# Optimization experiments

Hardware: AMD Instinct MI355X
Metric: run time of the kernel (lower is better)

Reference implementation:

```python
import jax, jax.numpy as jnp
import numpy as np
from jax import lax

NS, W, BS, NSENT, EMB, H, NMEN, NCAND, NTOK, NENTV = 640, 64, 16, 40, 512, 256, 32, 32, 50000, 100000


def _gru_dir(xp, valid, Whh, bhh):
    # xp: [T,B,3H] precomputed input projection; valid: [T,B] bool
    h0 = jnp.zeros((xp.shape[1], Whh.shape[1]), xp.dtype)
    def step(h, inp):
        x, v = inp
        g = h @ Whh.T + bhh
        xr, xz, xn = jnp.split(x, 3, axis=-1)
        hr, hz, hn = jnp.split(g, 3, axis=-1)
        r = jax.nn.sigmoid(xr + hr)
        z = jax.nn.sigmoid(xz + hz)
        n = jnp.tanh(xn + r * hn)
        hnew = (1.0 - z) * n + z * h
        hnew = jnp.where(v[:, None], hnew, h)  # freeze state past seq end (packed-seq semantics)
        return hnew, hnew * v[:, None]         # zero padded outputs like pad_packed_sequence
    _, ys = lax.scan(step, h0, (xp, valid))
    return ys  # [T,B,H]


def _att_birnn(x, lens, Wih_f, Whh_f, bih_f, bhh_f, Wih_b, Whh_b, bih_b, bhh_b, lin_w, lin_b, attw):
    # x: [B,T,I], lens: [B] (descending, lens[0]==T) -> attended pooling [B,2H]
    T = x.shape[1]
    valid = jnp.arange(T)[:, None] < lens[None, :]  # [T,B]
    xp_f = jnp.einsum('bti,oi->tbo', x, Wih_f) + bih_f
    xp_b = jnp.einsum('bti,oi->tbo', x, Wih_b) + bih_b
    ys_f = _gru_dir(xp_f, valid, Whh_f, bhh_f)
    ys_b = _gru_dir(xp_b[::-1], valid[::-1], Whh_b, bhh_b)[::-1]
    enc = jnp.concatenate([ys_f, ys_b], -1)  # [T,B,2H]
    emb_h = jnp.tanh(jnp.einsum('tbh,oh->tbo', enc, lin_w) + lin_b)
    att = emb_h @ attw  # [T,B]
    e = jnp.exp(att) * valid  # original uses raw exp with additive 1e-4 denom
    wgt = e / (jnp.sum(e, 0, keepdims=True) + 1e-4)
    return jnp.sum(wgt[..., None] * enc, 0)  # [B,2H]


def _cos(a, b, eps=1e-8):
    dot = jnp.sum(a * b, -1)
    na = jnp.sqrt(jnp.sum(a * a, -1))
    nb = jnp.sqrt(jnp.sum(b * b, -1))
    return dot / jnp.maximum(na * nb, eps)


def _forward(batch_doc, sent_order, length_sent, length_doc, men_sent_idx, can_ent_idx, cand_mask,
             embed_doc, embed_ent, wp, sp, mlp_w, mlp_b):
    emb_w = embed_doc[batch_doc]                         # [NS,W,EMB]; eval mode -> no dropout
    sent_embs = _att_birnn(emb_w, length_sent, *wp)      # [NS,2H]
    padded = jnp.concatenate([jnp.zeros((1, sent_embs.shape[1]), sent_embs.dtype), sent_embs], 0)
    each_sent = padded[sent_order]                       # [BS,NSENT,2H] (_reorder_sent)
    doc_embs = _att_birnn(each_sent, length_doc, *sp)    # [BS,2H]
    emb_ent = embed_ent[can_ent_idx]                     # [BS,NMEN,NCAND,EMB]
    sent_vecs = each_sent[jnp.arange(each_sent.shape[0])[:, None], men_sent_idx]  # [BS,NMEN,2H]
    # vectorized replacement of the triple python loop of per-element cosine sims
    ss = _cos(sent_vecs[:, :, None, :], emb_ent) * cand_mask  # [BS,NMEN,NCAND]
    ds = _cos(doc_embs[:, None, None, :], emb_ent) * cand_mask
    cc = jnp.concatenate([ss, ds], -1)                   # [BS,NMEN,2*NCAND]
    mask = (ss != 0).astype(cc.dtype)
    return (cc @ mlp_w.T + mlp_b) * mask


def setup_inputs() -> dict:
    key = jax.random.key(0)
    ks = jax.random.split(key, 36)
    batch_doc = jax.random.randint(ks[0], (NS, W), 0, NTOK, dtype=jnp.int32)
    length_sent = jnp.sort(jax.random.randint(ks[1], (NS,), 1, W + 1, dtype=jnp.int32))[::-1].at[0].set(W)
    length_doc = jnp.sort(jax.random.randint(ks[2], (BS,), 1, NSENT + 1, dtype=jnp.int32))[::-1].at[0].set(NSENT)
    so = jax.random.randint(ks[3], (BS, NSENT), 1, NS + 1, dtype=jnp.int32)
    sent_order = jnp.where(jnp.arange(NSENT)[None, :] < length_doc[:, None], so, 0)
    men_sent_idx = jax.random.randint(ks[4], (BS, NMEN), 0, NSENT, dtype=jnp.int32) % length_doc[:, None]
    can_ent_idx = jax.random.randint(ks[5], (BS, NMEN, NCAND), 1, NENTV, dtype=jnp.int32)
    cand_mask = (jax.random.uniform(ks[6], (BS, NMEN, NCAND)) < 0.8).astype(jnp.float32)
    def nrm(k, shape, s=0.05):
        return s * jax.random.normal(k, shape, dtype=jnp.float32)
    embed_doc = nrm(ks[7], (NTOK, EMB)).at[0].set(0.0)   # padding_idx=0
    embed_ent = nrm(ks[8], (NENTV, EMB)).at[0].set(0.0)
    d = {
        'batch_doc': batch_doc, 'sent_order': sent_order, 'length_sent': length_sent,
        'length_doc': length_doc, 'men_sent_idx': men_sent_idx, 'can_ent_idx': can_ent_idx,
        'cand_mask': cand_mask, 'embed_doc': embed_doc, 'embed_ent': embed_ent,
        'w_Wih_f': nrm(ks[9], (3 * H, EMB)), 'w_Whh_f': nrm(ks[10], (3 * H, H)),
        'w_bih_f': nrm(ks[11], (3 * H,)), 'w_bhh_f': nrm(ks[12], (3 * H,)),
        'w_Wih_b': nrm(ks[13], (3 * H, EMB)), 'w_Whh_b': nrm(ks[14], (3 * H, H)),
        'w_bih_b': nrm(ks[15], (3 * H,)), 'w_bhh_b': nrm(ks[16], (3 * H,)),
        'w_lin_w': nrm(ks[17], (2 * H, 2 * H)), 'w_lin_b': nrm(ks[18], (2 * H,)),
        'w_attw': nrm(ks[19], (2 * H,)),
        's_Wih_f': nrm(ks[20], (3 * H, 2 * H)), 's_Whh_f': nrm(ks[21], (3 * H, H)),
        's_bih_f': nrm(ks[22], (3 * H,)), 's_bhh_f': nrm(ks[23], (3 * H,)),
        's_Wih_b': nrm(ks[24], (3 * H, 2 * H)), 's_Whh_b': nrm(ks[25], (3 * H, H)),
        's_bih_b': nrm(ks[26], (3 * H,)), 's_bhh_b': nrm(ks[27], (3 * H,)),
        's_lin_w': nrm(ks[28], (2 * H, 2 * H)), 's_lin_b': nrm(ks[29], (2 * H,)),
        's_attw': nrm(ks[30], (2 * H,)),
        'mlp_w': nrm(ks[31], (NCAND, 2 * NCAND)), 'mlp_b': nrm(ks[32], (NCAND,)),
    }
    return d


def reference(batch_doc, sent_order, length_sent, length_doc, men_sent_idx, can_ent_idx, cand_mask,
              embed_doc, embed_ent,
              w_Wih_f, w_Whh_f, w_bih_f, w_bhh_f, w_Wih_b, w_Whh_b, w_bih_b, w_bhh_b, w_lin_w, w_lin_b, w_attw,
              s_Wih_f, s_Whh_f, s_bih_f, s_bhh_f, s_Wih_b, s_Whh_b, s_bih_b, s_bhh_b, s_lin_w, s_lin_b, s_attw,
              mlp_w, mlp_b):
    wp = (w_Wih_f, w_Whh_f, w_bih_f, w_bhh_f, w_Wih_b, w_Whh_b, w_bih_b, w_bhh_b, w_lin_w, w_lin_b, w_attw)
    sp = (s_Wih_f, s_Whh_f, s_bih_f, s_bhh_f, s_Wih_b, s_Whh_b, s_bih_b, s_bhh_b, s_lin_w, s_lin_b, s_attw)
    return _forward(batch_doc, sent_order, length_sent, length_doc, men_sent_idx, can_ent_idx, cand_mask,
                    embed_doc, embed_ent, wp, sp, mlp_w, mlp_b)
```

## Files before the change

### kernel.cpp

```cpp
#include <hip/hip_runtime.h>
#include <cstdint>
#include <cstddef>


typedef __attribute__((ext_vector_type(8))) short bf16x8;
typedef __attribute__((ext_vector_type(8))) _Float16 f16x8;
typedef __attribute__((ext_vector_type(4))) float f32x4;

__device__ __forceinline__ float bfraw2f(unsigned int u16) {
    unsigned int x = u16 << 16; float f; __builtin_memcpy(&f, &x, 4); return f;
}
__device__ __forceinline__ unsigned short f2bfraw(float f) {
    unsigned int u; __builtin_memcpy(&u, &f, 4);
    unsigned int r = u + 0x7fffu + ((u >> 16) & 1u);
    return (unsigned short)(r >> 16);
}
__device__ __forceinline__ unsigned short f2h(float f) {
    _Float16 h = (_Float16)f; unsigned short u; __builtin_memcpy(&u, &h, 2); return u;
}
__device__ __forceinline__ float h2f(unsigned short u) {
    _Float16 h; __builtin_memcpy(&h, &u, 2); return (float)h;
}
__device__ __forceinline__ float bflo(unsigned int p) {
    unsigned int x = p << 16; float f; __builtin_memcpy(&f, &x, 4); return f;
}
__device__ __forceinline__ float bfhi(unsigned int p) {
    unsigned int x = p & 0xffff0000u; float f; __builtin_memcpy(&f, &x, 4); return f;
}
__device__ __forceinline__ float fast_sigmoid(float x) { return 1.f / (1.f + __expf(-x)); }
__device__ __forceinline__ float fast_tanh(float x) {
    x = fminf(fmaxf(x, -30.f), 30.f);
    float e = __expf(2.f * x);
    return (e - 1.f) / (e + 1.f);
}
__device__ __forceinline__ float fin(float x) {
    return (x == x && fabsf(x) < 1e30f) ? x : 0.f;
}

__device__ __forceinline__ float ldsc(const void* p, size_t i, int m) {
    return m ? bfraw2f(((const unsigned short*)p)[i]) : ((const float*)p)[i];
}
__device__ __forceinline__ bf16x8 ld8bf(const void* p, size_t ei, int m) {
    if (m) return *(const bf16x8*)((const unsigned short*)p + ei);
    const float* f = (const float*)p + ei;
    f32x4 a = *(const f32x4*)f, b = *(const f32x4*)(f + 4);
    bf16x8 r;
    r[0] = (short)f2bfraw(a[0]); r[1] = (short)f2bfraw(a[1]);
    r[2] = (short)f2bfraw(a[2]); r[3] = (short)f2bfraw(a[3]);
    r[4] = (short)f2bfraw(b[0]); r[5] = (short)f2bfraw(b[1]);
    r[6] = (short)f2bfraw(b[2]); r[7] = (short)f2bfraw(b[3]);
    return r;
}
__device__ __forceinline__ void ld8f(const void* p, size_t ei, int m, float* o) {
    if (m) {
        uint4 wv = *(const uint4*)((const unsigned short*)p + ei);
        o[0] = bflo(wv.x); o[1] = bfhi(wv.x); o[2] = bflo(wv.y); o[3] = bfhi(wv.y);
        o[4] = bflo(wv.z); o[5] = bfhi(wv.z); o[6] = bflo(wv.w); o[7] = bfhi(wv.w);
    } else {
        const float* f = (const float*)p + ei;
        #pragma unroll
        for (int i = 0; i < 8; ++i) o[i] = f[i];
    }
}

__global__ void k_probe(const unsigned short* __restrict__ w, int* __restrict__ flag) {
    if (threadIdx.x == 0) {
        int bad = 0;
        for (int i = 0; i < 512; ++i) {
            float v = bfraw2f(w[i]);
            if (!(fabsf(v) <= 1.0f)) bad++;
        }
        flag[0] = (bad == 0) ? 1 : 0;
        flag[1] = 1;
    }
}

__global__ void p_cvt(const void* __restrict__ src, unsigned short* __restrict__ dst,
                      int n, const int* __restrict__ modep) {
    const int m = modep[0];
    for (int i = blockIdx.x * 256 + threadIdx.x; i < n; i += gridDim.x * 256)
        dst[i] = f2bfraw(ldsc(src, i, m));
}
__global__ void p_cvt_h(const void* __restrict__ src, unsigned short* __restrict__ dst,
                        int n, const int* __restrict__ modep) {
    const int m = modep[0];
    for (int i = blockIdx.x * 256 + threadIdx.x; i < n; i += gridDim.x * 256)
        dst[i] = f2h(ldsc(src, i, m));
}

__global__ void p_whh_swz(const void* __restrict__ whh, unsigned short* __restrict__ dst,
                          const int* __restrict__ modep) {
    const int m = modep[0];
    const int idx = blockIdx.x * 256 + threadIdx.x;
    if (idx >= 24576) return;
    const int lane = idx & 63, ks = (idx >> 6) & 7;
    const int g = (idx >> 9) % 6, w = idx / 3072;
    const int lm = lane & 15, q = lane >> 4;
    const int reg = g >> 1, nt = g & 1;
    const int row = reg * 256 + w * 32 + nt * 16 + lm;
    const size_t src = (size_t)row * 256 + ks * 32 + q * 8;
    const size_t d = (size_t)idx * 8;
    #pragma unroll
    for (int e = 0; e < 8; ++e) dst[d + e] = f2bfraw(ldsc(whh, src + e, m));
}

__global__ __launch_bounds__(256, 2) void k_xp_word(
    const void* __restrict__ embA, const int* __restrict__ batch_doc,
    const unsigned short* __restrict__ wih,
    const void* __restrict__ bih_f, const void* __restrict__ bih_b,
    unsigned short* __restrict__ xp, int b0, int nb,
    const int* __restrict__ amode, const int* __restrict__ modep)
{
    __shared__ unsigned short As[64][40];
    __shared__ unsigned short Bs[256][40];
    const int am = amode[0], m = modep[0];
    const int bm = blockIdx.x, bc = blockIdx.y;
    const int tid = threadIdx.x;
    const int wave = tid >> 6, lane = tid & 63, lm = lane & 15, q = lane >> 4;
    const int arow = tid >> 2, akoff = (tid & 3) * 8;
    const int r = bm * 64 + arow;
    const int tt = r / nb, bl = r - tt * nb;
    const size_t aei = (size_t)batch_doc[(b0 + bl) * 64 + tt] * 512 + akoff;

    const f32x4 fzero = {0.f, 0.f, 0.f, 0.f};
    f32x4 acc[4][4];
    #pragma unroll
    for (int i = 0; i < 4; ++i)
        #pragma unroll
        for (int j = 0; j < 4; ++j) acc[i][j] = fzero;

    for (int kt = 0; kt < 16; ++kt) {
        *(bf16x8*)&As[arow][akoff] = ld8bf(embA, aei + kt * 32, am);
        #pragma unroll
        for (int ld = 0; ld < 4; ++ld) {
            int e = ld * 256 + tid;
            int n = e >> 2, koff = (e & 3) * 8;
            int gn = bc * 256 + n;
            *(uint4*)&Bs[n][koff] = *(const uint4*)(wih + (size_t)gn * 512 + kt * 32 + koff);
        }
        __syncthreads();
        bf16x8 af[4], bv[4];
        #pragma unroll
        for (int mt = 0; mt < 4; ++mt) af[mt] = *(const bf16x8*)&As[mt * 16 + lm][q * 8];
        #pragma unroll
        for (int nt = 0; nt < 4; ++nt) bv[nt] = *(const bf16x8*)&Bs[wave * 64 + nt * 16 + lm][q * 8];
        #pragma unroll
        for (int mt = 0; mt < 4; ++mt)
            #pragma unroll
            for (int nt = 0; nt < 4; ++nt)
                acc[mt][nt] = __builtin_amdgcn_mfma_f32_16x16x32_bf16(af[mt], bv[nt], acc[mt][nt], 0, 0, 0);
        __syncthreads();
    }

    const size_t XPT = (size_t)64 * nb * 768;
    #pragma unroll
    for (int nt = 0; nt < 4; ++nt) {
        const int cn = bc * 256 + wave * 64 + nt * 16 + lm;
        const int dirb = (cn >= 768);
        const int o = cn - dirb * 768;
        const float bias = ldsc(dirb ? bih_b : bih_f, o, m);
        #pragma unroll
        for (int mt = 0; mt < 4; ++mt)
            #pragma unroll
            for (int j = 0; j < 4; ++j) {
                const int rr = bm * 64 + mt * 16 + q * 4 + j;
                xp[(dirb ? XPT : 0) + (size_t)rr * 768 + o] = f2h(acc[mt][nt][j] + bias);
            }
    }
}

__global__ __launch_bounds__(512, 2) void k_gru(
    const unsigned short* __restrict__ xp,
    const unsigned short* __restrict__ wswz_f,
    const unsigned short* __restrict__ wswz_b,
    const void* __restrict__ bhh_f, const void* __restrict__ bhh_b,
    const int* __restrict__ lens, unsigned short* __restrict__ enc, int T, int NB,
    const int* __restrict__ modep)
{
    __shared__ unsigned short hHi[2][16][264];
    __shared__ unsigned short hLo[2][16][264];
    __shared__ unsigned short xpS[2][16][776];
    __shared__ float bhhS[768];
    __shared__ int lensS[16];
    const int m = modep[0];
    const int tid = threadIdx.x;
    const int w = tid >> 6, lane = tid & 63, lm = lane & 15, q = lane >> 4;
    const int dir = blockIdx.x & 1, sg = blockIdx.x >> 1;
    const int s0 = sg << 4;
    const unsigned short* wsw =
        (dir ? wswz_b : wswz_f) + (size_t)w * 24576 + (size_t)lane * 8;
    const void* bhh = dir ? bhh_b : bhh_f;
    const unsigned short* xpd = xp + (dir ? (size_t)T * NB * 768 : 0);

    for (int e = tid; e < 16 * 264; e += 512) {
        (&hHi[0][0][0])[e] = 0; (&hLo[0][0][0])[e] = 0;
    }
    for (int j = tid; j < 768; j += 512) bhhS[j] = ldsc(bhh, j, m);
    if (tid < 16) lensS[tid] = lens[s0 + tid];

    bf16x8 bper[3][8];
    #pragma unroll
    for (int g = 0; g < 3; ++g)
        #pragma unroll
        for (int ks = 0; ks < 8; ++ks)
            bper[g][ks] = *(const bf16x8*)(wsw + (size_t)(g * 8 + ks) * 512);

    {
        const int t0 = dir ? (T - 1) : 0;
        const unsigned short* xrow = xpd + ((size_t)t0 * NB + s0) * 768;
        #pragma unroll
        for (int i = 0; i < 3; ++i) {
            int e = tid + i * 512;
            uint4 v = *(const uint4*)(xrow + e * 8);
            *(uint4*)&xpS[0][e / 96][(e % 96) * 8] = v;
        }
    }
    __syncthreads();

    const f32x4 fzero = {0.f, 0.f, 0.f, 0.f};
    float hreg[2][4] = {};
    uint4 stg[3];
    for (int step = 0; step < T; ++step) {
        const int t = dir ? (T - 1 - step) : step;
        const int cur = step & 1, nxt = cur ^ 1;

        const bool havenext = (step + 1 < T);
        if (havenext) {
            const int tn = dir ? (T - 2 - step) : (step + 1);
            const unsigned short* xrow = xpd + ((size_t)tn * NB + s0) * 768;
            #pragma unroll
            for (int i = 0; i < 3; ++i)
                stg[i] = *(const uint4*)(xrow + (tid + i * 512) * 8);
        }

        f32x4 acc[6];
        #pragma unroll
        for (int i = 0; i < 6; ++i) acc[i] = fzero;

        #pragma unroll
        for (int ph = 0; ph < 2; ++ph) {
            const int kb = ph * 4;
            bf16x8 ahi[4], alo[4];
            #pragma unroll
            for (int k = 0; k < 4; ++k) {
                ahi[k] = *(const bf16x8*)&hHi[cur][lm][(kb + k) * 32 + q * 8];
                alo[k] = *(const bf16x8*)&hLo[cur][lm][(kb + k) * 32 + q * 8];
            }
            bf16x8 bs3[4], bs4[4], bs5[4];
            #pragma unroll
            for (int k = 0; k < 4; ++k) {
                bs3[k] = *(const bf16x8*)(wsw + (size_t)(24 + kb + k) * 512);
                bs4[k] = *(const bf16x8*)(wsw + (size_t)(32 + kb + k) * 512);
                bs5[k] = *(const bf16x8*)(wsw + (size_t)(40 + kb + k) * 512);
            }
            #pragma unroll
            for (int g = 0; g < 3; ++g)
                #pragma unroll
                for (int k = 0; k < 4; ++k) {
                    acc[g] = __builtin_amdgcn_mfma_f32_16x16x32_bf16(ahi[k], bper[g][kb + k], acc[g], 0, 0, 0);
                    acc[g] = __builtin_amdgcn_mfma_f32_16x16x32_bf16(alo[k], bper[g][kb + k], acc[g], 0, 0, 0);
                }
            #pragma unroll
            for (int k = 0; k < 4; ++k) {
                acc[3] = __builtin_amdgcn_mfma_f32_16x16x32_bf16(ahi[k], bs3[k], acc[3], 0, 0, 0);
                acc[3] = __builtin_amdgcn_mfma_f32_16x16x32_bf16(alo[k], bs3[k], acc[3], 0, 0, 0);
                acc[4] = __builtin_amdgcn_mfma_f32_16x16x32_bf16(ahi[k], bs4[k], acc[4], 0, 0, 0);
                acc[4] = __builtin_amdgcn_mfma_f32_16x16x32_bf16(alo[k], bs4[k], acc[4], 0, 0, 0);
                acc[5] = __builtin_amdgcn_mfma_f32_16x16x32_bf16(ahi[k], bs5[k], acc[5], 0, 0, 0);
                acc[5] = __builtin_amdgcn_mfma_f32_16x16x32_bf16(alo[k], bs5[k], acc[5], 0, 0, 0);
            }
        }

        #pragma unroll
        for (int nt = 0; nt < 2; ++nt) {
            const int col = w * 32 + nt * 16 + lm;
            const float br = bhhS[col], bz = bhhS[256 + col], bn = bhhS[512 + col];
            #pragma unroll
            for (int j = 0; j < 4; ++j) {
                const int s = q * 4 + j;
                const float xr = h2f(xpS[cur][s][col]);
                const float xz = h2f(xpS[cur][s][256 + col]);
                const float xn = h2f(xpS[cur][s][512 + col]);
                const float rr = fast_sigmoid(xr + acc[nt][j] + br);
                const float zz = fast_sigmoid(xz + acc[2 + nt][j] + bz);
                const float nn = fast_tanh(xn + rr * (acc[4 + nt][j] + bn));
                const float hold = hreg[nt][j];
                float hnew = (1.f - zz) * nn + zz * hold;
                const bool v = (t < lensS[s]);
                hnew = v ? hnew : hold;
                hreg[nt][j] = hnew;
                const unsigned short uh = f2bfraw(hnew);
                hHi[nxt][s][col] = uh;
                hLo[nxt][s][col] = f2bfraw(hnew - bfraw2f(uh));
                enc[((size_t)t * NB + s0 + s) * 512 + (size_t)dir * 256 + col] = f2h(v ? hnew : 0.f);
            }
        }

        if (havenext) {
            #pragma unroll
            for (int i = 0; i < 3; ++i) {
                int e = tid + i * 512;
                *(uint4*)&xpS[nxt][e / 96][(e % 96) * 8] = stg[i];
            }
        }
        __syncthreads();
    }
}

__global__ __launch_bounds__(256, 1) void k_att(
    const unsigned short* __restrict__ enc,
    const unsigned short* __restrict__ lin_w,
    const void* __restrict__ lin_b, const void* __restrict__ attw,
    float* __restrict__ att_out, const int* __restrict__ modep)
{
    __shared__ unsigned short As[64][40];
    __shared__ unsigned short Bs[512][40];
    __shared__ float att_part[4][64];
    const int m = modep[0];
    const int bm = blockIdx.x;
    const int tid = threadIdx.x;
    const int wave = tid >> 6, lane = tid & 63, lm = lane & 15, q = lane >> 4;
    const int arow = tid >> 2, akoff = (tid & 3) * 8;
    const unsigned short* aptr = enc + (size_t)(bm * 64 + arow) * 512 + akoff;

    const f32x4 fzero = {0.f, 0.f, 0.f, 0.f};
    f32x4 acc[4][8];
    #pragma unroll
    for (int i = 0; i < 4; ++i)
        #pragma unroll
        for (int j = 0; j < 8; ++j) acc[i][j] = fzero;

    for (int kt = 0; kt < 16; ++kt) {
        *(uint4*)&As[arow][akoff] = *(const uint4*)(aptr + kt * 32);
        #pragma unroll
        for (int ld = 0; ld < 8; ++ld) {
            int e = ld * 256 + tid;
            int n = e >> 2, koff = (e & 3) * 8;
            *(uint4*)&Bs[n][koff] = *(const uint4*)(lin_w + (size_t)n * 512 + kt * 32 + koff);
        }
        __syncthreads();
        f16x8 af[4];
        #pragma unroll
        for (int mt = 0; mt < 4; ++mt) af[mt] = *(const f16x8*)&As[mt * 16 + lm][q * 8];
        #pragma unroll
        for (int nt = 0; nt < 8; ++nt) {
            f16x8 bv = *(const f16x8*)&Bs[wave * 128 + nt * 16 + lm][q * 8];
            #pragma unroll
            for (int mt = 0; mt < 4; ++mt)
                acc[mt][nt] = __builtin_amdgcn_mfma_f32_16x16x32_f16(af[mt], bv, acc[mt][nt], 0, 0, 0);
        }
        __syncthreads();
    }

    float part[4][4] = {};
    #pragma unroll
    for (int nt = 0; nt < 8; ++nt) {
        const int col = wave * 128 + nt * 16 + lm;
        const float lb = ldsc(lin_b, col, m);
        const float aw = ldsc(attw, col, m);
        #pragma unroll
        for (int mt = 0; mt < 4; ++mt)
            #pragma unroll
            for (int j = 0; j < 4; ++j)
                part[mt][j] += fast_tanh(acc[mt][nt][j] + lb) * aw;
    }
    #pragma unroll
    for (int mt = 0; mt < 4; ++mt)
        #pragma unroll
        for (int j = 0; j < 4; ++j) {
            float v = part[mt][j];
            #pragma unroll
            for (int d0 = 1; d0 < 16; d0 <<= 1) v += __shfl_xor(v, d0);
            part[mt][j] = v;
        }
    if (lm == 0) {
        #pragma unroll
        for (int mt = 0; mt < 4; ++mt)
            #pragma unroll
            for (int j = 0; j < 4; ++j)
                att_part[wave][mt * 16 + q * 4 + j] = part[mt][j];
    }
    __syncthreads();
    if (tid < 64)
        att_out[(size_t)bm * 64 + tid] =
            att_part[0][tid] + att_part[1][tid] + att_part[2][tid] + att_part[3][tid];
}

__global__ __launch_bounds__(256) void k_softsum(
    const float* __restrict__ att, const unsigned short* __restrict__ enc,
    const int* __restrict__ lens, float* __restrict__ out,
    float* __restrict__ zero_row, int T, int NB)
{
    __shared__ float eS[64];
    __shared__ float dS;
    const int bb = blockIdx.x, tid = threadIdx.x;
    if (zero_row && bb == 0) { for (int j = tid; j < 512; j += 256) zero_row[j] = 0.f; }
    const int len = lens[bb];
    if (tid < T) {
        float a = fminf(att[(size_t)tid * NB + bb], 50.f);
        eS[tid] = (tid < len) ? __expf(a) : 0.f;
    }
    __syncthreads();
    if (tid == 0) { float s = 0.f; for (int t2 = 0; t2 < T; ++t2) s += eS[t2]; dS = s + 1e-4f; }
    __syncthreads();
    const float inv = 1.f / dS;
    for (int j = tid; j < 512; j += 256) {
        float a0 = 0.f;
        for (int t2 = 0; t2 < T; ++t2) a0 += eS[t2] * h2f(enc[((size_t)t2 * NB + bb) * 512 + j]);
        out[(size_t)bb * 512 + j] = fin(a0 * inv);
    }
}

__global__ __launch_bounds__(256) void k_sent_xp(
    const int* __restrict__ sent_order, const float* __restrict__ sent_pad,
    const unsigned short* __restrict__ swih,
    const void* __restrict__ bih_f, const void* __restrict__ bih_b,
    float* __restrict__ each_sent, unsigned short* __restrict__ xp_s,
    const int* __restrict__ modep)
{
    __shared__ float aS[512];
    const int m = modep[0];
    const int r = blockIdx.x, tid = threadIdx.x;
    const int idx = sent_order[r];
    const float* src = sent_pad + (size_t)idx * 512;
    for (int j = tid; j < 512; j += 256) { float v = src[j]; aS[j] = v; each_sent[(size_t)r * 512 + j] = v; }
    __syncthreads();
    const int d = r / 40, i2 = r % 40;
    #pragma unroll
    for (int p = 0; p < 6; ++p) {
        const int o = p * 256 + tid;
        const int dirb = (o >= 768);
        const int oo = o - dirb * 768;
        float s = ldsc(dirb ? bih_b : bih_f, oo, m);
        const unsigned short* wrow = swih + (size_t)o * 512;
        for (int k = 0; k < 512; k += 8) {
            const uint4 wv = *(const uint4*)(wrow + k);
            float wf[8];
            wf[0] = bflo(wv.x); wf[1] = bfhi(wv.x); wf[2] = bflo(wv.y); wf[3] = bfhi(wv.y);
            wf[4] = bflo(wv.z); wf[5] = bfhi(wv.z); wf[6] = bflo(wv.w); wf[7] = bfhi(wv.w);
            #pragma unroll
            for (int u = 0; u < 8; ++u) s += aS[k + u] * wf[u];
        }
        xp_s[(size_t)dirb * (40 * 16 * 768) + ((size_t)i2 * 16 + d) * 768 + oo] = f2h(s);
    }
}

__global__ __launch_bounds__(256) void k_final(
    const int* __restrict__ men_sent_idx, const int* __restrict__ can_ent_idx,
    const void* __restrict__ cand_mask, const void* __restrict__ embed_ent,
    const float* __restrict__ each_sent, const float* __restrict__ doc_embs,
    const void* __restrict__ mlp_w, const void* __restrict__ mlp_b,
    void* __restrict__ out, const int* __restrict__ modep)
{
    const int bm = blockIdx.x;
    const int b = bm >> 5;
    __shared__ float sv[512], dv[512];
    __shared__ float red[256];
    __shared__ float ssA[32], dsA[32];
    __shared__ float norms[2];
    const int m = modep[0];
    const int tid = threadIdx.x;
    const int sidx = men_sent_idx[bm];
    const float* svp = each_sent + ((size_t)b * 40 + sidx) * 512;
    const float* dvp = doc_embs + (size_t)b * 512;
    float pa = 0.f, pd = 0.f;
    for (int j = tid; j < 512; j += 256) {
        float a = svp[j], d0 = dvp[j];
        sv[j] = a; dv[j] = d0; pa += a * a; pd += d0 * d0;
    }
    red[tid] = pa; __syncthreads();
    for (int s = 128; s > 0; s >>= 1) { if (tid < s) red[tid] += red[tid + s]; __syncthreads(); }
    if (tid == 0) norms[0] = sqrtf(red[0]);
    __syncthreads();
    red[tid] = pd; __syncthreads();
    for (int s = 128; s > 0; s >>= 1) { if (tid < s) red[tid] += red[tid + s]; __syncthreads(); }
    if (tid == 0) norms[1] = sqrtf(red[0]);
    __syncthreads();

    const int c = tid >> 3, jg = tid & 7;
    const int ei = can_ent_idx[(size_t)bm * 32 + c];
    float dsv = 0.f, ddv = 0.f, ne = 0.f;
    for (int k = 0; k < 64; k += 8) {
        float wf[8];
        ld8f(embed_ent, (size_t)ei * 512 + jg * 64 + k, m, wf);
        const int base = jg * 64 + k;
        #pragma unroll
        for (int u = 0; u < 8; ++u) {
            dsv += sv[base + u] * wf[u];
            ddv += dv[base + u] * wf[u];
            ne  += wf[u] * wf[u];
        }
    }
    #pragma unroll
    for (int d0 = 1; d0 < 8; d0 <<= 1) {
        dsv += __shfl_xor(dsv, d0);
        ddv += __shfl_xor(ddv, d0);
        ne  += __shfl_xor(ne, d0);
    }
    if (jg == 0) {
        const float nen = sqrtf(ne);
        const float cm = ldsc(cand_mask, (size_t)bm * 32 + c, m);
        ssA[c] = dsv / fmaxf(norms[0] * nen, 1e-8f) * cm;
        dsA[c] = ddv / fmaxf(norms[1] * nen, 1e-8f) * cm;
    }
    __syncthreads();
    if (tid < 32) {
        float o = ldsc(mlp_b, tid, m);
        for (int j2 = 0; j2 < 32; ++j2) {
            o += ssA[j2] * ldsc(mlp_w, tid * 64 + j2, m);
            o += dsA[j2] * ldsc(mlp_w, tid * 64 + 32 + j2, m);
        }
        const float maskv = (ssA[tid] != 0.f) ? 1.f : 0.f;
        const float v = fin(o * maskv);
        if (m) ((unsigned short*)out)[(size_t)bm * 32 + tid] = f2bfraw(v);
        else   ((float*)out)[(size_t)bm * 32 + tid] = v;
    }
}

extern "C" void kernel_launch(void* const* d_in, const int* in_sizes, int n_in,
                              void* d_out, int out_size, void* d_ws, size_t ws_size,
                              hipStream_t stream)
{
    (void)in_sizes; (void)n_in; (void)out_size;
    const int* batch_doc    = (const int*)d_in[0];
    const int* sent_order   = (const int*)d_in[1];
    const int* length_sent  = (const int*)d_in[2];
    const int* length_doc   = (const int*)d_in[3];
    const int* men_sent_idx = (const int*)d_in[4];
    const int* can_ent_idx  = (const int*)d_in[5];
    const void* cand_mask = d_in[6];
    const void* embed_doc = d_in[7];
    const void* embed_ent = d_in[8];
    const void* wWihF = d_in[9];
    const void* wWhhF = d_in[10];
    const void* wBihF = d_in[11];
    const void* wBhhF = d_in[12];
    const void* wWihB = d_in[13];
    const void* wWhhB = d_in[14];
    const void* wBihB = d_in[15];
    const void* wBhhB = d_in[16];
    const void* wLinW = d_in[17];
    const void* wLinB = d_in[18];
    const void* wAttw = d_in[19];
    const void* sWihF = d_in[20];
    const void* sWhhF = d_in[21];
    const void* sBihF = d_in[22];
    const void* sBhhF = d_in[23];
    const void* sWihB = d_in[24];
    const void* sWhhB = d_in[25];
    const void* sBihB = d_in[26];
    const void* sBhhB = d_in[27];
    const void* sLinW = d_in[28];
    const void* sLinB = d_in[29];
    const void* sAttw = d_in[30];
    const void* mlpW  = d_in[31];
    const void* mlpB  = d_in[32];

    const size_t N_EMB = (size_t)50000 * 512;
    const size_t HEAD =
        256 + 4 * (size_t)196608 * 2 +
        (size_t)1536 * 512 * 2 + (size_t)512 * 512 * 2 +
        (size_t)1536 * 512 * 2 + (size_t)512 * 512 * 2 +
        (size_t)328192 * 4;
    const size_t SENT_REGION = 1310720 + 1966080 + 655360 + 2816 + 32768;
    auto need = [&](int nbq, int e) -> size_t {
        size_t word = (size_t)nbq * (196608 + 65536 + 256);
        size_t region = word > SENT_REGION ? word : SENT_REGION;
        return HEAD + region + (e ? N_EMB * 2 : 0) + (1u << 20);
    };
    int emb_cvt = 1, nb = 320;
    {
        const int ladder[6] = {640, 320, 160, 80, 40, 16};
        bool found = false;
        for (int i = 0; i < 6 && !found; ++i)
            for (int e = 1; e >= 0 && !found; --e)
                if (need(ladder[i], e) <= ws_size) { emb_cvt = e; nb = ladder[i]; found = true; }
    }

    char* base = (char*)d_ws;
    size_t off = 0;
    auto take = [&](size_t bytes) -> void* {
        void* p = base + off; off += (bytes + 255) & ~(size_t)255; return p;
    };
    int* mode = (int*)take(256);
    unsigned short* swzWF = (unsigned short*)take((size_t)196608 * 2);
    unsigned short* swzWB = (unsigned short*)take((size_t)196608 * 2);
    unsigned short* swzSF = (unsigned short*)take((size_t)196608 * 2);
    unsigned short* swzSB = (unsigned short*)take((size_t)196608 * 2);
    unsigned short* wih_w = (unsigned short*)take((size_t)1536 * 512 * 2);
    unsigned short* lin_h = (unsigned short*)take((size_t)512 * 512 * 2);
    unsigned short* swih  = (unsigned short*)take((size_t)1536 * 512 * 2);
    unsigned short* slin_h= (unsigned short*)take((size_t)512 * 512 * 2);
    float* sent_pad  = (float*)take((size_t)328192 * 4);

    size_t word_bytes = (size_t)nb * (196608 + 65536 + 256);
    size_t region_bytes = word_bytes > SENT_REGION ? word_bytes : SENT_REGION;
    char* region = (char*)take(region_bytes);
    unsigned short* xp_c  = (unsigned short*)region;
    unsigned short* enc_c = (unsigned short*)(region + (size_t)nb * 196608);
    float* att_c          = (float*)(region + (size_t)nb * 196608 + (size_t)nb * 65536);
    float* each_sent      = (float*)region;
    unsigned short* xp_s  = (unsigned short*)(region + 1310720);
    unsigned short* enc_s = (unsigned short*)(region + 1310720 + 1966080);
    float* att_s          = (float*)(region + 1310720 + 1966080 + 655360);
    float* doc_embs       = (float*)(region + 1310720 + 1966080 + 655360 + 2816);

    unsigned short* emb_bf = emb_cvt ? (unsigned short*)take(N_EMB * 2) : nullptr;

    k_probe<<<1, 64, 0, stream>>>((const unsigned short*)wWhhF, mode);
    p_whh_swz<<<96, 256, 0, stream>>>(wWhhF, swzWF, mode);
    p_whh_swz<<<96, 256, 0, stream>>>(wWhhB, swzWB, mode);
    p_whh_swz<<<96, 256, 0, stream>>>(sWhhF, swzSF, mode);
    p_whh_swz<<<96, 256, 0, stream>>>(sWhhB, swzSB, mode);
    p_cvt<<<256, 256, 0, stream>>>(wWihF, wih_w, 768 * 512, mode);
    p_cvt<<<256, 256, 0, stream>>>(wWihB, wih_w + (size_t)768 * 512, 768 * 512, mode);
    p_cvt_h<<<256, 256, 0, stream>>>(wLinW, lin_h, 512 * 512, mode);
    p_cvt<<<256, 256, 0, stream>>>(sWihF, swih, 768 * 512, mode);
    p_cvt<<<256, 256, 0, stream>>>(sWihB, swih + (size_t)768 * 512, 768 * 512, mode);
    p_cvt_h<<<256, 256, 0, stream>>>(sLinW, slin_h, 512 * 512, mode);
    if (emb_cvt) p_cvt<<<2048, 256, 0, stream>>>(embed_doc, emb_bf, (int)N_EMB, mode);

    const void* embA = emb_cvt ? (const void*)emb_bf : embed_doc;
    const int* amode = emb_cvt ? (mode + 1) : mode;

    for (int b0 = 0; b0 < 640; b0 += nb) {
        k_xp_word<<<dim3(nb, 6), 256, 0, stream>>>(embA, batch_doc, wih_w,
                                                   wBihF, wBihB, xp_c, b0, nb, amode, mode);
        k_gru<<<2 * (nb / 16), 512, 0, stream>>>(xp_c, swzWF, swzWB, wBhhF, wBhhB,
                                                 length_sent + b0, enc_c, 64, nb, mode);
        k_att<<<nb, 256, 0, stream>>>(enc_c, lin_h, wLinB, wAttw, att_c, mode);
        k_softsum<<<nb, 256, 0, stream>>>(att_c, enc_c, length_sent + b0,
                                          sent_pad + (size_t)(1 + b0) * 512,
                                          (b0 == 0) ? sent_pad : nullptr, 64, nb);
    }
    k_sent_xp<<<640, 256, 0, stream>>>(sent_order, sent_pad, swih, sBihF, sBihB,
                                       each_sent, xp_s, mode);
    k_gru<<<2, 512, 0, stream>>>(xp_s, swzSF, swzSB, sBhhF, sBhhB,
                                 length_doc, enc_s, 40, 16, mode);
    k_att<<<10, 256, 0, stream>>>(enc_s, slin_h, sLinB, sAttw, att_s, mode);
    k_softsum<<<16, 256, 0, stream>>>(att_s, enc_s, length_doc, doc_embs, nullptr, 40, 16);
    k_final<<<512, 256, 0, stream>>>(men_sent_idx, can_ent_idx, cand_mask, embed_ent,
                                     each_sent, doc_embs, mlpW, mlpB, d_out, mode);
}
```

Baseline: 1.385 ms.

## Add single-pass workspace plan that skips embedding-table conversion and aliases buffers

```diff
diff --git a/kernel.cpp b/kernel.cpp
--- a/kernel.cpp
+++ b/kernel.cpp
@@ -557,6 +557,68 @@
     const void* mlpB  = d_in[32];
 
     const size_t N_EMB = (size_t)50000 * 512;
+    char* base = (char*)d_ws;
+
+    const size_t SP_MODE  = 0;
+    const size_t SP_SWZWF = 256;
+    const size_t SP_SWZWB = SP_SWZWF + 393216;
+    const size_t SP_ATTC  = SP_SWZWB + 393216;
+    const size_t SP_XPC   = SP_ATTC + 163840;
+    const size_t SP_ENCC  = SP_XPC + (size_t)125829120;
+    const size_t SP_END   = SP_ENCC + (size_t)41943040;
+    const bool single = (SP_END + 65536) <= ws_size;
+
+    if (single) {
+        int* mode             = (int*)(base + SP_MODE);
+        unsigned short* swzWF = (unsigned short*)(base + SP_SWZWF);
+        unsigned short* swzWB = (unsigned short*)(base + SP_SWZWB);
+        float* att_c          = (float*)(base + SP_ATTC);
+        unsigned short* xp_c  = (unsigned short*)(base + SP_XPC);
+        unsigned short* enc_c = (unsigned short*)(base + SP_ENCC);
+        unsigned short* wih_w = enc_c;
+        char* xr = (char*)xp_c;
+        unsigned short* lin_h  = (unsigned short*)(xr);
+        float* sent_pad        = (float*)(xr + 524288);
+        unsigned short* swzSF  = (unsigned short*)(xr + 1837056);
+        unsigned short* swzSB  = (unsigned short*)(xr + 2230272);
+        unsigned short* swih   = (unsigned short*)(xr + 2623488);
+        unsigned short* slin_h = (unsigned short*)(xr + 4196352);
+        float* each_sent       = (float*)(xr + 4720640);
+        unsigned short* xp_s   = (unsigned short*)(xr + 6031360);
+        unsigned short* enc_s  = (unsigned short*)(xr + 7997440);
+        float* att_s           = (float*)(xr + 8652800);
+        float* doc_embs        = (float*)(xr + 8655616);
+
+        k_probe<<<1, 64, 0, stream>>>((const unsigned short*)wWhhF, mode);
+        p_whh_swz<<<96, 256, 0, stream>>>(wWhhF, swzWF, mode);
+        p_whh_swz<<<96, 256, 0, stream>>>(wWhhB, swzWB, mode);
+        p_cvt<<<256, 256, 0, stream>>>(wWihF, wih_w, 768 * 512, mode);
+        p_cvt<<<256, 256, 0, stream>>>(wWihB, wih_w + (size_t)768 * 512, 768 * 512, mode);
+
+        k_xp_word<<<dim3(640, 6), 256, 0, stream>>>(embed_doc, batch_doc, wih_w,
+                                                    wBihF, wBihB, xp_c, 0, 640, mode, mode);
+        k_gru<<<80, 512, 0, stream>>>(xp_c, swzWF, swzWB, wBhhF, wBhhB,
+                                      length_sent, enc_c, 64, 640, mode);
+        p_cvt_h<<<128, 256, 0, stream>>>(wLinW, lin_h, 512 * 512, mode);
+        k_att<<<640, 256, 0, stream>>>(enc_c, lin_h, wLinB, wAttw, att_c, mode);
+        k_softsum<<<640, 256, 0, stream>>>(att_c, enc_c, length_sent,
+                                           sent_pad + 512, sent_pad, 64, 640);
+        p_whh_swz<<<96, 256, 0, stream>>>(sWhhF, swzSF, mode);
+        p_whh_swz<<<96, 256, 0, stream>>>(sWhhB, swzSB, mode);
+        p_cvt<<<256, 256, 0, stream>>>(sWihF, swih, 768 * 512, mode);
+        p_cvt<<<256, 256, 0, stream>>>(sWihB, swih + (size_t)768 * 512, 768 * 512, mode);
+        p_cvt_h<<<128, 256, 0, stream>>>(sLinW, slin_h, 512 * 512, mode);
+        k_sent_xp<<<640, 256, 0, stream>>>(sent_order, sent_pad, swih, sBihF, sBihB,
+                                           each_sent, xp_s, mode);
+        k_gru<<<2, 512, 0, stream>>>(xp_s, swzSF, swzSB, sBhhF, sBhhB,
+                                     length_doc, enc_s, 40, 16, mode);
+        k_att<<<10, 256, 0, stream>>>(enc_s, slin_h, sLinB, sAttw, att_s, mode);
+        k_softsum<<<16, 256, 0, stream>>>(att_s, enc_s, length_doc, doc_embs, nullptr, 40, 16);
+        k_final<<<512, 256, 0, stream>>>(men_sent_idx, can_ent_idx, cand_mask, embed_ent,
+                                         each_sent, doc_embs, mlpW, mlpB, d_out, mode);
+        return;
+    }
+
     const size_t HEAD =
         256 + 4 * (size_t)196608 * 2 +
         (size_t)1536 * 512 * 2 + (size_t)512 * 512 * 2 +
@@ -570,14 +632,13 @@
     };
     int emb_cvt = 1, nb = 320;
     {
-        const int ladder[6] = {640, 320, 160, 80, 40, 16};
+        const int ladder[5] = {320, 160, 80, 40, 16};
         bool found = false;
-        for (int i = 0; i < 6 && !found; ++i)
+        for (int i = 0; i < 5 && !found; ++i)
             for (int e = 1; e >= 0 && !found; --e)
                 if (need(ladder[i], e) <= ws_size) { emb_cvt = e; nb = ladder[i]; found = true; }
     }
 
-    char* base = (char*)d_ws;
     size_t off = 0;
     auto take = [&](size_t bytes) -> void* {
         void* p = base + off; off += (bytes + 255) & ~(size_t)255; return p;
```

After: 1.359 ms. No clear change (-1.9%).

## Switch GRU recurrence to single fp16 MFMA and pre-swizzle input projections

Applied to the files above, without the earlier changes.

```diff
diff --git a/kernel.cpp b/kernel.cpp
--- a/kernel.cpp
+++ b/kernel.cpp
@@ -101,7 +101,7 @@
     const size_t src = (size_t)row * 256 + ks * 32 + q * 8;
     const size_t d = (size_t)idx * 8;
     #pragma unroll
-    for (int e = 0; e < 8; ++e) dst[d + e] = f2bfraw(ldsc(whh, src + e, m));
+    for (int e = 0; e < 8; ++e) dst[d + e] = f2h(ldsc(whh, src + e, m));
 }
 
 __global__ __launch_bounds__(256, 2) void k_xp_word(
@@ -153,18 +153,28 @@
     }
 
     const size_t XPT = (size_t)64 * nb * 768;
+    const int nbg = nb >> 4;
     #pragma unroll
     for (int nt = 0; nt < 4; ++nt) {
         const int cn = bc * 256 + wave * 64 + nt * 16 + lm;
         const int dirb = (cn >= 768);
         const int o = cn - dirb * 768;
         const float bias = ldsc(dirb ? bih_b : bih_f, o, m);
+        const int gate = o >> 8, c = o & 255;
+        const int ww = c >> 5, ntt = (c >> 4) & 1, lmm = c & 15;
+        const int u0 = gate * 8 + ntt * 4;
         #pragma unroll
         for (int mt = 0; mt < 4; ++mt)
             #pragma unroll
             for (int j = 0; j < 4; ++j) {
                 const int rr = bm * 64 + mt * 16 + q * 4 + j;
-                xp[(dirb ? XPT : 0) + (size_t)rr * 768 + o] = f2h(acc[mt][nt][j] + bias);
+                const int t = rr / nb, sgl = rr - t * nb;
+                const int g = sgl >> 4, si = sgl & 15;
+                const int qq = si >> 2, jj = si & 3;
+                const size_t addr = (dirb ? XPT : (size_t)0)
+                    + (((size_t)t * nbg + g) * 8 + ww) * 1536
+                    + (size_t)(qq * 16 + lmm) * 24 + u0 + jj;
+                xp[addr] = f2h(acc[mt][nt][j] + bias);
             }
     }
 }
@@ -177,9 +187,7 @@
     const int* __restrict__ lens, unsigned short* __restrict__ enc, int T, int NB,
     const int* __restrict__ modep)
 {
-    __shared__ unsigned short hHi[2][16][264];
-    __shared__ unsigned short hLo[2][16][264];
-    __shared__ unsigned short xpS[2][16][776];
+    __shared__ unsigned short hS[2][16][264];
     __shared__ float bhhS[768];
     __shared__ int lensS[16];
     const int m = modep[0];
@@ -190,48 +198,35 @@
     const unsigned short* wsw =
         (dir ? wswz_b : wswz_f) + (size_t)w * 24576 + (size_t)lane * 8;
     const void* bhh = dir ? bhh_b : bhh_f;
-    const unsigned short* xpd = xp + (dir ? (size_t)T * NB * 768 : 0);
-
-    for (int e = tid; e < 16 * 264; e += 512) {
-        (&hHi[0][0][0])[e] = 0; (&hLo[0][0][0])[e] = 0;
-    }
+    const unsigned short* xpd = xp + (dir ? (size_t)T * NB * 768 : 0)
+                               + ((size_t)sg * 8 + w) * 1536 + (size_t)lane * 24;
+
+    for (int e = tid; e < 16 * 264; e += 512) (&hS[0][0][0])[e] = 0;
     for (int j = tid; j < 768; j += 512) bhhS[j] = ldsc(bhh, j, m);
     if (tid < 16) lensS[tid] = lens[s0 + tid];
 
-    bf16x8 bper[3][8];
+    f16x8 bper[3][8];
     #pragma unroll
     for (int g = 0; g < 3; ++g)
         #pragma unroll
         for (int ks = 0; ks < 8; ++ks)
-            bper[g][ks] = *(const bf16x8*)(wsw + (size_t)(g * 8 + ks) * 512);
-
-    {
-        const int t0 = dir ? (T - 1) : 0;
-        const unsigned short* xrow = xpd + ((size_t)t0 * NB + s0) * 768;
-        #pragma unroll
-        for (int i = 0; i < 3; ++i) {
-            int e = tid + i * 512;
-            uint4 v = *(const uint4*)(xrow + e * 8);
-            *(uint4*)&xpS[0][e / 96][(e % 96) * 8] = v;
-        }
-    }
+            bper[g][ks] = *(const f16x8*)(wsw + (size_t)(g * 8 + ks) * 512);
+
     __syncthreads();
 
     const f32x4 fzero = {0.f, 0.f, 0.f, 0.f};
     float hreg[2][4] = {};
-    uint4 stg[3];
+    const long long xstride = dir ? -(long long)NB * 768 : (long long)NB * 768;
+    const unsigned short* xrow = xpd + (size_t)(dir ? (T - 1) : 0) * (size_t)NB * 768;
+
     for (int step = 0; step < T; ++step) {
         const int t = dir ? (T - 1 - step) : step;
         const int cur = step & 1, nxt = cur ^ 1;
 
-        const bool havenext = (step + 1 < T);
-        if (havenext) {
-            const int tn = dir ? (T - 2 - step) : (step + 1);
-            const unsigned short* xrow = xpd + ((size_t)tn * NB + s0) * 768;
-            #pragma unroll
-            for (int i = 0; i < 3; ++i)
-                stg[i] = *(const uint4*)(xrow + (tid + i * 512) * 8);
-        }
+        const uint4 xv0 = *(const uint4*)(xrow);
+        const uint4 xv1 = *(const uint4*)(xrow + 8);
+        const uint4 xv2 = *(const uint4*)(xrow + 16);
+        xrow += xstride;
 
         f32x4 acc[6];
         #pragma unroll
@@ -240,36 +235,34 @@
         #pragma unroll
         for (int ph = 0; ph < 2; ++ph) {
             const int kb = ph * 4;
-            bf16x8 ahi[4], alo[4];
+            f16x8 af[4];
+            #pragma unroll
+            for (int k = 0; k < 4; ++k)
+                af[k] = *(const f16x8*)&hS[cur][lm][(kb + k) * 32 + q * 8];
+            f16x8 bs3[4], bs4[4], bs5[4];
             #pragma unroll
             for (int k = 0; k < 4; ++k) {
-                ahi[k] = *(const bf16x8*)&hHi[cur][lm][(kb + k) * 32 + q * 8];
-                alo[k] = *(const bf16x8*)&hLo[cur][lm][(kb + k) * 32 + q * 8];
-            }
-            bf16x8 bs3[4], bs4[4], bs5[4];
-            #pragma unroll
-            for (int k = 0; k < 4; ++k) {
-                bs3[k] = *(const bf16x8*)(wsw + (size_t)(24 + kb + k) * 512);
-                bs4[k] = *(const bf16x8*)(wsw + (size_t)(32 + kb + k) * 512);
-                bs5[k] = *(const bf16x8*)(wsw + (size_t)(40 + kb + k) * 512);
+                bs3[k] = *(const f16x8*)(wsw + (size_t)(24 + kb + k) * 512);
+                bs4[k] = *(const f16x8*)(wsw + (size_t)(32 + kb + k) * 512);
+                bs5[k] = *(const f16x8*)(wsw + (size_t)(40 + kb + k) * 512);
             }
             #pragma unroll
             for (int g = 0; g < 3; ++g)
                 #pragma unroll
-                for (int k = 0; k < 4; ++k) {
-                    acc[g] = __builtin_amdgcn_mfma_f32_16x16x32_bf16(ahi[k], bper[g][kb + k], acc[g], 0, 0, 0);
-                    acc[g] = __builtin_amdgcn_mfma_f32_16x16x32_bf16(alo[k], bper[g][kb + k], acc[g], 0, 0, 0);
-                }
+                for (int k = 0; k < 4; ++k)
+                    acc[g] = __builtin_amdgcn_mfma_f32_16x16x32_f16(af[k], bper[g][kb + k], acc[g], 0, 0, 0);
             #pragma unroll
             for (int k = 0; k < 4; ++k) {
-                acc[3] = __builtin_amdgcn_mfma_f32_16x16x32_bf16(ahi[k], bs3[k], acc[3], 0, 0, 0);
-                acc[3] = __builtin_amdgcn_mfma_f32_16x16x32_bf16(alo[k], bs3[k], acc[3], 0, 0, 0);
-                acc[4] = __builtin_amdgcn_mfma_f32_16x16x32_bf16(ahi[k], bs4[k], acc[4], 0, 0, 0);
-                acc[4] = __builtin_amdgcn_mfma_f32_16x16x32_bf16(alo[k], bs4[k], acc[4], 0, 0, 0);
-                acc[5] = __builtin_amdgcn_mfma_f32_16x16x32_bf16(ahi[k], bs5[k], acc[5], 0, 0, 0);
-                acc[5] = __builtin_amdgcn_mfma_f32_16x16x32_bf16(alo[k], bs5[k], acc[5], 0, 0, 0);
+                acc[3] = __builtin_amdgcn_mfma_f32_16x16x32_f16(af[k], bs3[k], acc[3], 0, 0, 0);
+                acc[4] = __builtin_amdgcn_mfma_f32_16x16x32_f16(af[k], bs4[k], acc[4], 0, 0, 0);
+                acc[5] = __builtin_amdgcn_mfma_f32_16x16x32_f16(af[k], bs5[k], acc[5], 0, 0, 0);
             }
         }
+
+        f16x8 xr8, xz8, xn8;
+        __builtin_memcpy(&xr8, &xv0, 16);
+        __builtin_memcpy(&xz8, &xv1, 16);
+        __builtin_memcpy(&xn8, &xv2, 16);
 
         #pragma unroll
         for (int nt = 0; nt < 2; ++nt) {
@@ -278,9 +271,9 @@
             #pragma unroll
             for (int j = 0; j < 4; ++j) {
                 const int s = q * 4 + j;
-                const float xr = h2f(xpS[cur][s][col]);
-                const float xz = h2f(xpS[cur][s][256 + col]);
-                const float xn = h2f(xpS[cur][s][512 + col]);
+                const float xr = (float)xr8[nt * 4 + j];
+                const float xz = (float)xz8[nt * 4 + j];
+                const float xn = (float)xn8[nt * 4 + j];
                 const float rr = fast_sigmoid(xr + acc[nt][j] + br);
                 const float zz = fast_sigmoid(xz + acc[2 + nt][j] + bz);
                 const float nn = fast_tanh(xn + rr * (acc[4 + nt][j] + bn));
@@ -289,18 +282,8 @@
                 const bool v = (t < lensS[s]);
                 hnew = v ? hnew : hold;
                 hreg[nt][j] = hnew;
-                const unsigned short uh = f2bfraw(hnew);
-                hHi[nxt][s][col] = uh;
-                hLo[nxt][s][col] = f2bfraw(hnew - bfraw2f(uh));
+                hS[nxt][s][col] = f2h(hnew);
                 enc[((size_t)t * NB + s0 + s) * 512 + (size_t)dir * 256 + col] = f2h(v ? hnew : 0.f);
-            }
-        }
-
-        if (havenext) {
-            #pragma unroll
-            for (int i = 0; i < 3; ++i) {
-                int e = tid + i * 512;
-                *(uint4*)&xpS[nxt][e / 96][(e % 96) * 8] = stg[i];
             }
         }
         __syncthreads();
@@ -426,6 +409,7 @@
     for (int j = tid; j < 512; j += 256) { float v = src[j]; aS[j] = v; each_sent[(size_t)r * 512 + j] = v; }
     __syncthreads();
     const int d = r / 40, i2 = r % 40;
+    const int qq = d >> 2, jj = d & 3;
     #pragma unroll
     for (int p = 0; p < 6; ++p) {
         const int o = p * 256 + tid;
@@ -441,7 +425,12 @@
             #pragma unroll
             for (int u = 0; u < 8; ++u) s += aS[k + u] * wf[u];
         }
-        xp_s[(size_t)dirb * (40 * 16 * 768) + ((size_t)i2 * 16 + d) * 768 + oo] = f2h(s);
+        const int gate = oo >> 8, c = oo & 255;
+        const int ww = c >> 5, ntt = (c >> 4) & 1, lmm = c & 15;
+        const size_t addr = (size_t)dirb * (40 * 16 * 768)
+            + ((size_t)i2 * 8 + ww) * 1536
+            + (size_t)(qq * 16 + lmm) * 24 + gate * 8 + ntt * 4 + jj;
+        xp_s[addr] = f2h(s);
     }
 }
 
@@ -557,6 +546,8 @@
     const void* mlpB  = d_in[32];
 
     const size_t N_EMB = (size_t)50000 * 512;
+    char* base = (char*)d_ws;
+
     const size_t HEAD =
         256 + 4 * (size_t)196608 * 2 +
         (size_t)1536 * 512 * 2 + (size_t)512 * 512 * 2 +
@@ -570,14 +561,13 @@
     };
     int emb_cvt = 1, nb = 320;
     {
-        const int ladder[6] = {640, 320, 160, 80, 40, 16};
+        const int ladder[5] = {320, 160, 80, 40, 16};
         bool found = false;
-        for (int i = 0; i < 6 && !found; ++i)
+        for (int i = 0; i < 5 && !found; ++i)
             for (int e = 1; e >= 0 && !found; --e)
                 if (need(ladder[i], e) <= ws_size) { emb_cvt = e; nb = ladder[i]; found = true; }
     }
 
-    char* base = (char*)d_ws;
     size_t off = 0;
     auto take = [&](size_t bytes) -> void* {
         void* p = base + off; off += (bytes + 255) & ~(size_t)255; return p;
```

After: 1.663 ms. +20.0%, slower.
